# Kernel tuning notes

Hardware: AMD Instinct MI355X
Metric: run time of the kernel (lower is better)

The kernel has to match this reference:

```python
import jax, jax.numpy as jnp
import numpy as np

N_CLASS = 5      # episode way
SHOTS = 5        # support images per class
D = 64           # local descriptor dim (feature_dim)
H = W = 16       # feature map spatial size
N_QUERY = 75     # 15 queries per class


def setup_inputs() -> dict:
    key = jax.random.key(0)
    k1, k2 = jax.random.split(key)
    support = jax.random.normal(k1, (N_CLASS * SHOTS, D, H, W), dtype=jnp.float32)
    query = jax.random.normal(k2, (N_QUERY, D, H, W), dtype=jnp.float32)
    return {"support": support, "query": query, "task_index": 0, "k": 3, "k2": 64}


def reference(support, query, task_index, k, k2):
    C = N_CLASS
    n, d, h, w = support.shape
    hw = h * w
    ns = n // C  # shots per class

    # Per-class support descriptors: [C, ns*h*w, d], L2-normalized along d
    s = support.reshape(C, ns, d, hw)
    s = jnp.transpose(s, (0, 1, 3, 2)).reshape(C, ns * hw, d)
    s = s / jnp.linalg.norm(s, axis=-1, keepdims=True)

    # Query local descriptors: [B, d, Nq], L2-normalized along d
    B = query.shape[0]
    q = query.reshape(B, d, -1)
    q = q / jnp.linalg.norm(q, axis=1, keepdims=True)

    # Cosine similarity per class: [C, B, Nq, M]  (M = ns*h*w support descriptors)
    sim = jnp.einsum('cmd,bdq->cbqm', s, q)

    # torch.topk(sim, k, dim=1): top-k over support descriptors M per query location
    v = jax.lax.top_k(sim, k)[0]          # [C, B, Nq, k]
    v = jnp.swapaxes(v, 2, 3)             # [C, B, k, Nq]
    # torch.topk(., k2, dim=2): top-k2 over query locations
    v = jax.lax.top_k(v, k2)[0]           # [C, B, k, k2]

    # cat over classes, unsqueeze, then view(-1, 1, k, k2)
    return v.reshape(-1, 1, k, k2)        # [C*B, 1, k, k2]
```

## Files before the change

kernel.cpp:

```cpp
#include <hip/hip_runtime.h>
#include <stdint.h>


#define C_CLS 5
#define SHOTS 5
#define DIM 64
#define HW 256
#define NQ 75
#define K1 3
#define K2 64
#define M_TOT 1280
#define MHALF 640
#define TROWS 128
#define NIT (MHALF / TROWS)
#define QG 2

using bf16x8 = __attribute__((ext_vector_type(8))) short;
using u32x4  = __attribute__((ext_vector_type(4))) unsigned int;
using f32x4  = __attribute__((ext_vector_type(4))) float;

typedef __attribute__((address_space(1))) const unsigned int GU32;
typedef __attribute__((address_space(3))) unsigned int LU32;

__device__ __forceinline__ void gload16(const void* g, void* l) {
    __builtin_amdgcn_global_load_lds((GU32*)g, (LU32*)l, 16, 0, 0);
}

__device__ inline unsigned short f2bf(float x) {
    uint32_t u = __float_as_uint(x);
    u += 0x7FFF + ((u >> 16) & 1);
    return (unsigned short)(u >> 16);
}

__device__ __forceinline__ void ins3(float v, float& t0, float& t1, float& t2) {
    t2 = __builtin_amdgcn_fmed3f(v, t1, t2);
    t1 = __builtin_amdgcn_fmed3f(v, t0, t1);
    t0 = fmaxf(t0, v);
}

__global__ __launch_bounds__(256)
void prep(const float* __restrict__ support, const float* __restrict__ query,
          unsigned short* __restrict__ Sn, unsigned short* __restrict__ Qn) {
    const int tid  = threadIdx.x;
    const int wv   = tid >> 6, lane = tid & 63;
    const int dg   = lane >> 4, dl = lane & 15;
    const int bid  = blockIdx.x;
    const float* src;
    unsigned short* dstblk;
    if (bid < NQ * 4) {
        const int b    = bid >> 2;
        const int desc = (bid & 3) * 64 + wv * 16 + dl;
        src    = query + (size_t)b * DIM * HW + desc;
        dstblk = Qn + (size_t)b * 16384 + (size_t)((bid & 3) * 4 + wv) * 1024;
    } else {
        const int sb   = bid - NQ * 4;
        const int cs   = sb >> 2;
        const int desc = (sb & 3) * 64 + wv * 16 + dl;
        const int c = cs / SHOTS, s = cs % SHOTS;
        src    = support + (size_t)cs * DIM * HW + desc;
        dstblk = Sn + (size_t)c * 81920 + (size_t)(s * 16 + (sb & 3) * 4 + wv) * 1024;
    }
    float v[16];
    float nrm = 0.f;
#pragma unroll
    for (int i = 0; i < 16; ++i) {
        const float x = src[(dg * 16 + i) * HW];
        v[i] = x; nrm = fmaf(x, x, nrm);
    }
    nrm += __shfl_xor(nrm, 16, 64);
    nrm += __shfl_xor(nrm, 32, 64);
    const float inv = rsqrtf(nrm);
    uint32_t p[8];
#pragma unroll
    for (int j = 0; j < 8; ++j)
        p[j] = (uint32_t)f2bf(v[2 * j] * inv) | ((uint32_t)f2bf(v[2 * j + 1] * inv) << 16);
    const int ck = dg >> 1;
#pragma unroll
    for (int q = 0; q < 2; ++q) {
        const int kg = (dg & 1) * 2 + q;
        uint4 wq = {p[q * 4 + 0], p[q * 4 + 1], p[q * 4 + 2], p[q * 4 + 3]};
        *(uint4*)(dstblk + ck * 512 + (kg * 16 + dl) * 8) = wq;
    }
}

__global__ __launch_bounds__(512)
void dn4_mfma(const unsigned short* __restrict__ Sn,
              const unsigned short* __restrict__ Qn,
              float* __restrict__ partial) {
    __shared__ unsigned short sB[2][TROWS * DIM];

    const int tid  = threadIdx.x;
    const int lane = tid & 63, w = tid >> 6;
    const int c15  = lane & 15, kg = lane >> 4;
    const int bid  = blockIdx.x;
    const int half = bid & 1;
    const int cb   = bid >> 1;
    const int c    = cb / NQ, b = cb % NQ;

    bf16x8 aq[QG][2];
    const unsigned short* qf = Qn + (size_t)b * 16384 + (size_t)(w * 2) * 1024;
#pragma unroll
    for (int g = 0; g < QG; ++g)
#pragma unroll
        for (int ck = 0; ck < 2; ++ck)
            aq[g][ck] = __builtin_bit_cast(bf16x8,
                *(const u32x4*)(qf + g * 1024 + ck * 512 + lane * 8));

    float t0[QG][4], t1[QG][4], t2[QG][4];
#pragma unroll
    for (int g = 0; g < QG; ++g)
#pragma unroll
        for (int r = 0; r < 4; ++r) { t0[g][r] = -2.f; t1[g][r] = -2.f; t2[g][r] = -2.f; }

    const f32x4 Z = {0.f, 0.f, 0.f, 0.f};
    const char* tb0 = (const char*)(Sn + (size_t)c * 81920 + (size_t)half * 40960);

#pragma unroll
    for (int rep = 0; rep < 2; ++rep)
        gload16(tb0 + rep * 8192 + tid * 16, (char*)sB[0] + rep * 8192 + w * 1024);
    __syncthreads();

    int cur = 0;
    for (int it = 0; it < NIT; ++it) {
        if (it < NIT - 1) {
            const char* tb = tb0 + (size_t)(it + 1) * 16384;
#pragma unroll
            for (int rep = 0; rep < 2; ++rep)
                gload16(tb + rep * 8192 + tid * 16,
                        (char*)sB[cur ^ 1] + rep * 8192 + w * 1024);
        }
#pragma unroll
        for (int ns = 0; ns < 8; ++ns) {
            const unsigned short* rp = &sB[cur][ns * 1024 + lane * 8];
            const bf16x8 b0 = __builtin_bit_cast(bf16x8, *(const u32x4*)rp);
            const bf16x8 b1 = __builtin_bit_cast(bf16x8, *(const u32x4*)(rp + 512));
#pragma unroll
            for (int g = 0; g < QG; ++g) {
                f32x4 acc = __builtin_amdgcn_mfma_f32_16x16x32_bf16(aq[g][0], b0, Z, 0, 0, 0);
                acc = __builtin_amdgcn_mfma_f32_16x16x32_bf16(aq[g][1], b1, acc, 0, 0, 0);
#pragma unroll
                for (int r = 0; r < 4; ++r)
                    ins3(acc[r], t0[g][r], t1[g][r], t2[g][r]);
            }
        }
        __syncthreads();
        cur ^= 1;
    }

#pragma unroll
    for (int g = 0; g < QG; ++g)
#pragma unroll
        for (int r = 0; r < 4; ++r)
#pragma unroll
            for (int off = 1; off < 16; off <<= 1) {
                const float o0 = __shfl_xor(t0[g][r], off, 64);
                const float o1 = __shfl_xor(t1[g][r], off, 64);
                const float o2 = __shfl_xor(t2[g][r], off, 64);
                ins3(o0, t0[g][r], t1[g][r], t2[g][r]);
                ins3(o1, t0[g][r], t1[g][r], t2[g][r]);
                ins3(o2, t0[g][r], t1[g][r], t2[g][r]);
            }

    if (c15 == 0) {
        float* pbase = partial + ((size_t)(cb * 2 + half) * K1) * HW;
#pragma unroll
        for (int g = 0; g < QG; ++g)
#pragma unroll
            for (int r = 0; r < 4; ++r) {
                const int qloc = (w * 2 + g) * 16 + kg * 4 + r;
                pbase[qloc]          = t0[g][r];
                pbase[HW + qloc]     = t1[g][r];
                pbase[2 * HW + qloc] = t2[g][r];
            }
    }
}

__global__ __launch_bounds__(256)
void dn4_topq(const float* __restrict__ partial, float* __restrict__ out) {
    __shared__ float sbuf[HW];
    const int tid = threadIdx.x;
    const int bid = blockIdx.x;
    const int ki  = bid % K1;
    const int cb  = bid / K1;

    const float* p = partial + (size_t)cb * 2 * K1 * HW + tid;
    float t0 = -2.f, t1 = -2.f, t2 = -2.f;
#pragma unroll
    for (int h = 0; h < 2; ++h)
#pragma unroll
        for (int r = 0; r < K1; ++r)
            ins3(p[(h * K1 + r) * HW], t0, t1, t2);
    float v = (ki == 0) ? t0 : (ki == 1) ? t1 : t2;

#pragma unroll
    for (int kk = 2; kk <= HW; kk <<= 1) {
#pragma unroll
        for (int j = kk >> 1; j > 0; j >>= 1) {
            const bool keep_max = (((tid & kk) == 0) == ((tid & j) == 0));
            float wv;
            if (j >= 64) {
                sbuf[tid] = v;
                __syncthreads();
                wv = sbuf[tid ^ j];
                __syncthreads();
            } else {
                wv = __shfl_xor(v, j, 64);
            }
            v = keep_max ? fmaxf(v, wv) : fminf(v, wv);
        }
    }
    if (tid < K2) out[(size_t)cb * K1 * K2 + (size_t)ki * K2 + tid] = v;
}

extern "C" void kernel_launch(void* const* d_in, const int* in_sizes, int n_in,
                              void* d_out, int out_size, void* d_ws, size_t ws_size,
                              hipStream_t stream) {
    const float* support = (const float*)d_in[0];
    const float* query   = (const float*)d_in[1];
    float* out = (float*)d_out;

    char* ws = (char*)d_ws;
    unsigned short* Sn = (unsigned short*)ws;
    unsigned short* Qn = (unsigned short*)(ws + 819200);
    float* partial     = (float*)(ws + 819200 + 2457600);

    prep    <<<dim3(400),              dim3(256), 0, stream>>>(support, query, Sn, Qn);
    dn4_mfma<<<dim3(C_CLS * NQ * 2),   dim3(512), 0, stream>>>(Sn, Qn, partial);
    dn4_topq<<<dim3(C_CLS * NQ * K1),  dim3(256), 0, stream>>>(partial, out);
}
```

Measured before the change: 51.87 us.

## Split support into quarters, stream tiles via registers, store bf16 partials

The MFMA kernel now splits each class's support descriptors into four quarters instead of two. It uses 256-thread blocks where each wave handles four query groups, and each lane loads its support fragments directly from global memory into registers with one-step prefetch, replacing the LDS double buffer and barriers. The top-3 merge after the shuffle reduction uses a cheaper sorted-merge formula, and partial results are stored as bf16 to cut traffic into the final top-k kernel. Storing partials in bf16 truncates values, so the output loses precision, and the final kernel must merge twice as many partials.

```diff
diff --git a/kernel.cpp b/kernel.cpp
--- a/kernel.cpp
+++ b/kernel.cpp
@@ -10,21 +10,13 @@
 #define K1 3
 #define K2 64
 #define M_TOT 1280
-#define MHALF 640
-#define TROWS 128
-#define NIT (MHALF / TROWS)
-#define QG 2
+#define MQ 4
+#define NSTEP 20
+#define QG 4
 
 using bf16x8 = __attribute__((ext_vector_type(8))) short;
 using u32x4  = __attribute__((ext_vector_type(4))) unsigned int;
 using f32x4  = __attribute__((ext_vector_type(4))) float;
-
-typedef __attribute__((address_space(1))) const unsigned int GU32;
-typedef __attribute__((address_space(3))) unsigned int LU32;
-
-__device__ __forceinline__ void gload16(const void* g, void* l) {
-    __builtin_amdgcn_global_load_lds((GU32*)g, (LU32*)l, 16, 0, 0);
-}
 
 __device__ inline unsigned short f2bf(float x) {
     uint32_t u = __float_as_uint(x);
@@ -83,22 +75,20 @@
     }
 }
 
-__global__ __launch_bounds__(512)
+__global__ __launch_bounds__(256)
 void dn4_mfma(const unsigned short* __restrict__ Sn,
               const unsigned short* __restrict__ Qn,
-              float* __restrict__ partial) {
-    __shared__ unsigned short sB[2][TROWS * DIM];
-
+              unsigned short* __restrict__ partial) {
     const int tid  = threadIdx.x;
     const int lane = tid & 63, w = tid >> 6;
     const int c15  = lane & 15, kg = lane >> 4;
     const int bid  = blockIdx.x;
-    const int half = bid & 1;
-    const int cb   = bid >> 1;
-    const int c    = cb / NQ, b = cb % NQ;
+    const int b    = bid % NQ;
+    const int cq   = bid / NQ;
+    const int c    = cq >> 2, qt = cq & 3;
 
     bf16x8 aq[QG][2];
-    const unsigned short* qf = Qn + (size_t)b * 16384 + (size_t)(w * 2) * 1024;
+    const unsigned short* qf = Qn + (size_t)b * 16384 + (size_t)(w * QG) * 1024;
 #pragma unroll
     for (int g = 0; g < QG; ++g)
 #pragma unroll
@@ -113,38 +103,29 @@
         for (int r = 0; r < 4; ++r) { t0[g][r] = -2.f; t1[g][r] = -2.f; t2[g][r] = -2.f; }
 
     const f32x4 Z = {0.f, 0.f, 0.f, 0.f};
-    const char* tb0 = (const char*)(Sn + (size_t)c * 81920 + (size_t)half * 40960);
-
-#pragma unroll
-    for (int rep = 0; rep < 2; ++rep)
-        gload16(tb0 + rep * 8192 + tid * 16, (char*)sB[0] + rep * 8192 + w * 1024);
-    __syncthreads();
-
-    int cur = 0;
-    for (int it = 0; it < NIT; ++it) {
-        if (it < NIT - 1) {
-            const char* tb = tb0 + (size_t)(it + 1) * 16384;
-#pragma unroll
-            for (int rep = 0; rep < 2; ++rep)
-                gload16(tb + rep * 8192 + tid * 16,
-                        (char*)sB[cur ^ 1] + rep * 8192 + w * 1024);
-        }
-#pragma unroll
-        for (int ns = 0; ns < 8; ++ns) {
-            const unsigned short* rp = &sB[cur][ns * 1024 + lane * 8];
-            const bf16x8 b0 = __builtin_bit_cast(bf16x8, *(const u32x4*)rp);
-            const bf16x8 b1 = __builtin_bit_cast(bf16x8, *(const u32x4*)(rp + 512));
-#pragma unroll
-            for (int g = 0; g < QG; ++g) {
-                f32x4 acc = __builtin_amdgcn_mfma_f32_16x16x32_bf16(aq[g][0], b0, Z, 0, 0, 0);
-                acc = __builtin_amdgcn_mfma_f32_16x16x32_bf16(aq[g][1], b1, acc, 0, 0, 0);
-#pragma unroll
-                for (int r = 0; r < 4; ++r)
-                    ins3(acc[r], t0[g][r], t1[g][r], t2[g][r]);
-            }
-        }
-        __syncthreads();
-        cur ^= 1;
+    const unsigned short* sp = Sn + (size_t)c * 81920 + (size_t)qt * (NSTEP * 1024);
+
+    u32x4 p0 = *(const u32x4*)(sp + lane * 8);
+    u32x4 p1 = *(const u32x4*)(sp + 512 + lane * 8);
+#pragma unroll
+    for (int it = 0; it < NSTEP; ++it) {
+        u32x4 n0 = p0, n1 = p1;
+        if (it + 1 < NSTEP) {
+            const unsigned short* rp = sp + (it + 1) * 1024 + lane * 8;
+            n0 = *(const u32x4*)rp;
+            n1 = *(const u32x4*)(rp + 512);
+        }
+        const bf16x8 b0 = __builtin_bit_cast(bf16x8, p0);
+        const bf16x8 b1 = __builtin_bit_cast(bf16x8, p1);
+#pragma unroll
+        for (int g = 0; g < QG; ++g) {
+            f32x4 acc = __builtin_amdgcn_mfma_f32_16x16x32_bf16(aq[g][0], b0, Z, 0, 0, 0);
+            acc = __builtin_amdgcn_mfma_f32_16x16x32_bf16(aq[g][1], b1, acc, 0, 0, 0);
+#pragma unroll
+            for (int r = 0; r < 4; ++r)
+                ins3(acc[r], t0[g][r], t1[g][r], t2[g][r]);
+        }
+        p0 = n0; p1 = n1;
     }
 
 #pragma unroll
@@ -156,40 +137,46 @@
                 const float o0 = __shfl_xor(t0[g][r], off, 64);
                 const float o1 = __shfl_xor(t1[g][r], off, 64);
                 const float o2 = __shfl_xor(t2[g][r], off, 64);
-                ins3(o0, t0[g][r], t1[g][r], t2[g][r]);
-                ins3(o1, t0[g][r], t1[g][r], t2[g][r]);
-                ins3(o2, t0[g][r], t1[g][r], t2[g][r]);
+                const float x = fmaxf(t0[g][r], o2);
+                const float y = fmaxf(t1[g][r], o1);
+                const float z = fmaxf(t2[g][r], o0);
+                t0[g][r] = fmaxf(fmaxf(x, y), z);
+                t1[g][r] = __builtin_amdgcn_fmed3f(x, y, z);
+                t2[g][r] = fminf(fminf(x, y), z);
             }
 
     if (c15 == 0) {
-        float* pbase = partial + ((size_t)(cb * 2 + half) * K1) * HW;
+        unsigned short* pbase =
+            partial + (((size_t)(c * NQ + b) * MQ + qt) * K1) * HW;
 #pragma unroll
         for (int g = 0; g < QG; ++g)
 #pragma unroll
             for (int r = 0; r < 4; ++r) {
-                const int qloc = (w * 2 + g) * 16 + kg * 4 + r;
-                pbase[qloc]          = t0[g][r];
-                pbase[HW + qloc]     = t1[g][r];
-                pbase[2 * HW + qloc] = t2[g][r];
+                const int qloc = (w * QG + g) * 16 + kg * 4 + r;
+                pbase[qloc]          = f2bf(t0[g][r]);
+                pbase[HW + qloc]     = f2bf(t1[g][r]);
+                pbase[2 * HW + qloc] = f2bf(t2[g][r]);
             }
     }
 }
 
 __global__ __launch_bounds__(256)
-void dn4_topq(const float* __restrict__ partial, float* __restrict__ out) {
+void dn4_topq(const unsigned short* __restrict__ partial, float* __restrict__ out) {
     __shared__ float sbuf[HW];
     const int tid = threadIdx.x;
     const int bid = blockIdx.x;
     const int ki  = bid % K1;
     const int cb  = bid / K1;
 
-    const float* p = partial + (size_t)cb * 2 * K1 * HW + tid;
+    const unsigned short* p = partial + (size_t)cb * MQ * K1 * HW + tid;
     float t0 = -2.f, t1 = -2.f, t2 = -2.f;
 #pragma unroll
-    for (int h = 0; h < 2; ++h)
-#pragma unroll
-        for (int r = 0; r < K1; ++r)
-            ins3(p[(h * K1 + r) * HW], t0, t1, t2);
+    for (int h = 0; h < MQ; ++h)
+#pragma unroll
+        for (int r = 0; r < K1; ++r) {
+            const float v = __uint_as_float((uint32_t)p[(h * K1 + r) * HW] << 16);
+            ins3(v, t0, t1, t2);
+        }
     float v = (ki == 0) ? t0 : (ki == 1) ? t1 : t2;
 
 #pragma unroll
@@ -220,11 +207,11 @@
     float* out = (float*)d_out;
 
     char* ws = (char*)d_ws;
-    unsigned short* Sn = (unsigned short*)ws;
-    unsigned short* Qn = (unsigned short*)(ws + 819200);
-    float* partial     = (float*)(ws + 819200 + 2457600);
+    unsigned short* Sn      = (unsigned short*)ws;
+    unsigned short* Qn      = (unsigned short*)(ws + 819200);
+    unsigned short* partial = (unsigned short*)(ws + 819200 + 2457600);
 
     prep    <<<dim3(400),              dim3(256), 0, stream>>>(support, query, Sn, Qn);
-    dn4_mfma<<<dim3(C_CLS * NQ * 2),   dim3(512), 0, stream>>>(Sn, Qn, partial);
+    dn4_mfma<<<dim3(C_CLS * MQ * NQ),  dim3(256), 0, stream>>>(Sn, Qn, partial);
     dn4_topq<<<dim3(C_CLS * NQ * K1),  dim3(256), 0, stream>>>(partial, out);
 }
```

New measurement: 51.25 us. No clear change (-1.2%).
